# Kernel tuning notes

Hardware: AMD Instinct MI355X
Metric: run time of the kernel (lower is better)

Reference implementation:

```python
import jax, jax.numpy as jnp
import numpy as np
import math

B, S, N, D_IN = 32, 60, 25, 100
GRU, TEMB, SEMB, SEM_IN, CH, OUT, NH = 512, 512, 512, 768, 256, 512, 8


def _ln(x, g, b, eps=1e-5):
    m = jnp.mean(x, axis=-1, keepdims=True)
    v = jnp.mean((x - m) ** 2, axis=-1, keepdims=True)
    return (x - m) * jax.lax.rsqrt(v + eps) * g + b


def _gru_dir(x, w_ih, w_hh, b_ih, b_hh, reverse):
    # x: [BN, S, F]; PyTorch GRU gate order (r, z, n); returns final hidden [BN, H]
    H = w_hh.shape[1]
    gi_all = jnp.einsum('bsf,gf->bsg', x, w_ih) + b_ih  # precompute input-side gates

    def step(h, gi):
        gh = h @ w_hh.T + b_hh
        i_r, i_z, i_n = jnp.split(gi, 3, axis=-1)
        h_r, h_z, h_n = jnp.split(gh, 3, axis=-1)
        r = jax.nn.sigmoid(i_r + h_r)
        z = jax.nn.sigmoid(i_z + h_z)
        n = jnp.tanh(i_n + r * h_n)
        h_new = (1.0 - z) * n + z * h
        return h_new, None

    h0 = jnp.zeros((x.shape[0], H), x.dtype)
    h_last, _ = jax.lax.scan(step, h0, jnp.swapaxes(gi_all, 0, 1), reverse=reverse)
    return h_last


def _forward(x, seq1_w1, seq1_b1, seq1_w2, seq1_b2, ln2_g, ln2_b,
             gru_wih_f, gru_whh_f, gru_bih_f, gru_bhh_f,
             gru_wih_b, gru_whh_b, gru_bih_b, gru_bhh_b,
             ln_g, ln_b, attn_in_w, attn_in_b, fc_ta_w, fc_ta_b,
             ln3_g, ln3_b, semantic_embs, sem_w, sem_b, lnsem_g, lnsem_b,
             att_alpha, dist_adj,
             gcn_w0, gcn_b0, gcn_w1, gcn_b1, gcn_w2, gcn_b2,
             gln1_g, gln1_b, gln2_g, gln2_b,
             enc_ln_g, enc_ln_b, fc_w, fc_b):
    Bx, Sx, Nx, _ = x.shape
    # --- latent_correlation_layer ---
    xr = jnp.transpose(x, (0, 2, 1, 3)).reshape(Bx * Nx, Sx, -1)  # [BN,S,D]
    h = jax.nn.relu(xr @ seq1_w1 + seq1_b1)
    h = jax.nn.relu(h @ seq1_w2 + seq1_b2)  # dropout p=0
    h = _ln(h, ln2_g, ln2_b)  # [BN,S,512]
    hf = _gru_dir(h, gru_wih_f, gru_whh_f, gru_bih_f, gru_bhh_f, False)
    hb = _gru_dir(h, gru_wih_b, gru_whh_b, gru_bih_b, gru_bhh_b, True)
    hn = jnp.concatenate([hf, hb], axis=-1).reshape(Bx, Nx, 2 * GRU)
    hn = _ln(hn, ln_g, ln_b)  # [B,N,2*GRU]
    # multihead self-attention weights (averaged over heads, then over batch)
    hd = (2 * GRU) // NH
    qkv = hn @ attn_in_w.T + attn_in_b
    q, k, _v = jnp.split(qkv, 3, axis=-1)
    q = q.reshape(Bx, Nx, NH, hd)
    k = k.reshape(Bx, Nx, NH, hd)
    scores = jnp.einsum('bihd,bjhd->bhij', q, k) / math.sqrt(hd)
    attention = jax.nn.softmax(scores, axis=-1).mean(axis=1).mean(axis=0)  # [N,N]
    # --- node features ---
    wr = jax.nn.relu(hn @ fc_ta_w + fc_ta_b)
    X = _ln(wr, ln3_g, ln3_b)  # [B,N,TEMB]
    te = _ln(semantic_embs @ sem_w + sem_b, lnsem_g, lnsem_b)  # [N,SEMB]
    X = jnp.concatenate([X, jnp.broadcast_to(te, (Bx,) + te.shape)], axis=-1)  # [B,N,TEMB+SEMB]
    # cosine-similarity embedding attention (same for every batch element)
    en = te / jnp.maximum(jnp.linalg.norm(te, axis=-1, keepdims=True), 1e-8)
    embed_att = en @ en.T  # [N,N]
    attention = (att_alpha * dist_adj + (1.0 - att_alpha) * embed_att) * attention
    # case-amplification mask (detached in the original -> stop_gradient)
    m = jax.lax.stop_gradient(attention)
    m = jnp.maximum(m, 0.0) ** 2.5
    m = m / jnp.max(m)
    mask = (m >= 0.08).astype(x.dtype)
    adj = attention * mask
    # --- GCN block (GCNConv, add_self_loops=False, normalize=False, dense adjacency) ---
    def gcn(Xin, W, b):
        # out[i] = sum_j adj[j,i] * (Xin[j] @ W) + b  (source->target flow)
        return jnp.einsum('ji,bjf->bif', adj, Xin @ W) + b
    Xg = jax.nn.relu(gcn(X, gcn_w0, gcn_b0))
    Xg = jax.nn.relu(_ln(gcn(Xg, gcn_w1, gcn_b1) + Xg, gln1_g, gln1_b))
    Xg = jax.nn.relu(_ln(gcn(Xg, gcn_w2, gcn_b2) + Xg, gln2_g, gln2_b))
    # --- encoder head ---
    Xg = _ln(Xg, enc_ln_g, enc_ln_b)
    X_hat = jax.nn.relu(jnp.concatenate([X, Xg], axis=-1) @ fc_w + fc_b)  # [B,N,OUT]
    return X_hat


def setup_inputs():
    key = jax.random.key(0)
    c = [0]

    def nrm(shape, scale=1.0):
        c[0] += 1
        return (jax.random.normal(jax.random.fold_in(key, c[0]), shape) * scale).astype(jnp.float32)

    z = lambda *s: jnp.zeros(s, jnp.float32)
    o = lambda *s: jnp.ones(s, jnp.float32)
    FDIM = TEMB + SEMB
    d = {
        'x': nrm((B, S, N, D_IN)),
        'seq1_w1': nrm((D_IN, 256), 0.06), 'seq1_b1': z(256),
        'seq1_w2': nrm((256, 512), 0.05), 'seq1_b2': z(512),
        'ln2_g': o(512), 'ln2_b': z(512),
        'gru_wih_f': nrm((3 * GRU, 512), 0.04), 'gru_whh_f': nrm((3 * GRU, GRU), 0.04),
        'gru_bih_f': z(3 * GRU), 'gru_bhh_f': z(3 * GRU),
        'gru_wih_b': nrm((3 * GRU, 512), 0.04), 'gru_whh_b': nrm((3 * GRU, GRU), 0.04),
        'gru_bih_b': z(3 * GRU), 'gru_bhh_b': z(3 * GRU),
        'ln_g': o(2 * GRU), 'ln_b': z(2 * GRU),
        'attn_in_w': nrm((3 * 2 * GRU, 2 * GRU), 0.03), 'attn_in_b': z(3 * 2 * GRU),
        'fc_ta_w': nrm((2 * GRU, TEMB), 0.04), 'fc_ta_b': z(TEMB),
        'ln3_g': o(TEMB), 'ln3_b': z(TEMB),
        'semantic_embs': nrm((N, SEM_IN)),
        'sem_w': nrm((SEM_IN, SEMB), 0.04), 'sem_b': z(SEMB),
        'lnsem_g': o(SEMB), 'lnsem_b': z(SEMB),
        'att_alpha': jnp.float32(0.5),
        'dist_adj': jax.random.uniform(jax.random.fold_in(key, 1000), (N, N), jnp.float32),
        'gcn_w0': nrm((FDIM, CH), 0.04), 'gcn_b0': z(CH),
        'gcn_w1': nrm((CH, CH), 0.06), 'gcn_b1': z(CH),
        'gcn_w2': nrm((CH, CH), 0.06), 'gcn_b2': z(CH),
        'gln1_g': o(CH), 'gln1_b': z(CH),
        'gln2_g': o(CH), 'gln2_b': z(CH),
        'enc_ln_g': o(CH), 'enc_ln_b': z(CH),
        'fc_w': nrm((FDIM + CH, OUT), 0.04), 'fc_b': z(OUT),
    }
    return d


def reference(x, seq1_w1, seq1_b1, seq1_w2, seq1_b2, ln2_g, ln2_b,
              gru_wih_f, gru_whh_f, gru_bih_f, gru_bhh_f,
              gru_wih_b, gru_whh_b, gru_bih_b, gru_bhh_b,
              ln_g, ln_b, attn_in_w, attn_in_b, fc_ta_w, fc_ta_b,
              ln3_g, ln3_b, semantic_embs, sem_w, sem_b, lnsem_g, lnsem_b,
              att_alpha, dist_adj,
              gcn_w0, gcn_b0, gcn_w1, gcn_b1, gcn_w2, gcn_b2,
              gln1_g, gln1_b, gln2_g, gln2_b,
              enc_ln_g, enc_ln_b, fc_w, fc_b):
    return _forward(x, seq1_w1, seq1_b1, seq1_w2, seq1_b2, ln2_g, ln2_b,
                    gru_wih_f, gru_whh_f, gru_bih_f, gru_bhh_f,
                    gru_wih_b, gru_whh_b, gru_bih_b, gru_bhh_b,
                    ln_g, ln_b, attn_in_w, attn_in_b, fc_ta_w, fc_ta_b,
                    ln3_g, ln3_b, semantic_embs, sem_w, sem_b, lnsem_g, lnsem_b,
                    att_alpha, dist_adj,
                    gcn_w0, gcn_b0, gcn_w1, gcn_b1, gcn_w2, gcn_b2,
                    gln1_g, gln1_b, gln2_g, gln2_b,
                    enc_ln_g, enc_ln_b, fc_w, fc_b)
```

## Files before the change

### kernel.cpp

```cpp
#include <hip/hip_runtime.h>
#include <hip/hip_bf16.h>
#include <math.h>

#define BB 32
#define SS 60
#define NN_ 25
#define DIN 100
#define BN 800
#define GRU_H 512
#define FDIM 1024
#define CH 256
#define OUTD 512

typedef unsigned short ushort_t;
typedef unsigned int u32;
typedef unsigned long long u64;
typedef float f32x4 __attribute__((ext_vector_type(4)));
typedef __bf16 bf16x8 __attribute__((ext_vector_type(8)));
typedef short s16x8 __attribute__((ext_vector_type(8)));

static const size_t O_HSEQB = 0;
static const size_t O_WB    = 12288000;
static const size_t O_HF32  = 13860864;
static const size_t O_HRING = 14680064;
static const size_t O_HN    = 15908864;
static const size_t O_QKV   = 16728064;
static const size_t O_SC    = 18366464;
static const size_t O_ADJ   = 18530304;
static const size_t O_WR    = 18530944;
static const size_t O_TEP   = 18940544;
static const size_t O_TE    = 18953344;
static const size_t O_XCAT  = 18966144;
static const size_t O_GTMP  = 19990144;
static const size_t O_XG0   = 20194944;
static const size_t O_XG1   = 20399744;
static const size_t O_XG2   = 20604544;
static const size_t O_W1TB  = 20809344;
static const size_t O_W2TB  = 20825728;
static const size_t O_AWB   = 20891264;
static const size_t O_FTWB  = 21939840;
static const size_t O_SMWB  = 22201984;
static const size_t O_G0WB  = 22398592;
static const size_t O_G1WB  = 22529664;
static const size_t O_G2WB  = 22562432;
static const size_t O_FCWB  = 22595200;
static const size_t O_FLAGS = 22922880;

__device__ __forceinline__ ushort_t f2b(float v)
{
  __hip_bfloat16 b = __float2bfloat16(v);
  return *reinterpret_cast<ushort_t*>(&b);
}

__device__ __forceinline__ float sig_fast(float v)
{
  return 1.f / (1.f + __expf(-v));
}
__device__ __forceinline__ float tanh_fast(float v)
{
  return 1.f - 2.f / (1.f + __expf(2.f * v));
}

__device__ __forceinline__ void block_reduce2(float& s, float& q, float* scratch)
{
  __syncthreads();
  #pragma unroll
  for (int off = 32; off > 0; off >>= 1) {
    s += __shfl_down(s, off);
    q += __shfl_down(q, off);
  }
  int tid = threadIdx.x;
  int w = tid >> 6;
  if ((tid & 63) == 0) { scratch[w * 2] = s; scratch[w * 2 + 1] = q; }
  __syncthreads();
  if (tid == 0) {
    float ss = 0.f, qq = 0.f;
    int nw = blockDim.x >> 6;
    for (int i = 0; i < nw; i++) { ss += scratch[i * 2]; qq += scratch[i * 2 + 1]; }
    scratch[0] = ss; scratch[1] = qq;
  }
  __syncthreads();
  s = scratch[0]; q = scratch[1];
}

__global__ __launch_bounds__(256) void k_cvt_plain_all(
    const float* __restrict__ wih_f, const float* __restrict__ whh_f,
    const float* __restrict__ wih_b, const float* __restrict__ whh_b,
    const float* __restrict__ attn_w,
    ushort_t* __restrict__ wb, ushort_t* __restrict__ awb)
{
  int i = blockIdx.x * 256 + threadIdx.x;
  wb[i]           = f2b(wih_f[i]);
  wb[786432 + i]  = f2b(whh_f[i]);
  wb[1572864 + i] = f2b(wih_b[i]);
  wb[2359296 + i] = f2b(whh_b[i]);
  awb[i]          = f2b(attn_w[i]);
  awb[786432 + i] = f2b(attn_w[786432 + i]);
  int j = 1572864 + i;
  if (j < 2097152) awb[j] = f2b(attn_w[j]);
}

struct TJob {
  const float* src; ushort_t* dst;
  int K, N, KP, base;
};

__global__ __launch_bounds__(256) void k_cvt_t_all(
    TJob j0, TJob j1, TJob j2, TJob j3, TJob j4, TJob j5, TJob j6, TJob j7)
{
  __shared__ float tile[32][33];
  int t = blockIdx.x;
  TJob jb = j0;
  if (t >= j7.base) jb = j7;
  else if (t >= j6.base) jb = j6;
  else if (t >= j5.base) jb = j5;
  else if (t >= j4.base) jb = j4;
  else if (t >= j3.base) jb = j3;
  else if (t >= j2.base) jb = j2;
  else if (t >= j1.base) jb = j1;
  int local = t - jb.base;
  int ktiles = (jb.KP + 31) >> 5;
  int n0 = (local / ktiles) * 32;
  int k0 = (local % ktiles) * 32;
  int tx = threadIdx.x & 31, ty = threadIdx.x >> 5;
  #pragma unroll
  for (int i = 0; i < 4; i++) {
    int k = k0 + ty + i * 8, n = n0 + tx;
    tile[ty + i * 8][tx] = (k < jb.K && n < jb.N) ? jb.src[(size_t)k * jb.N + n] : 0.f;
  }
  __syncthreads();
  #pragma unroll
  for (int i = 0; i < 4; i++) {
    int n = n0 + ty + i * 8, k = k0 + tx;
    if (n < jb.N && k < jb.KP) jb.dst[(size_t)n * jb.KP + k] = f2b(tile[tx][ty + i * 8]);
  }
}

__global__ __launch_bounds__(256, 1) void k_mlp_fused(
    const float* __restrict__ x,
    const ushort_t* __restrict__ w1tb,
    const float* __restrict__ b1,
    const ushort_t* __restrict__ w2tb,
    const float* __restrict__ b2,
    const float* __restrict__ g, const float* __restrict__ be,
    ushort_t* __restrict__ hseqb)
{
  __shared__ __align__(16) ushort_t xb[64][136];
  __shared__ __align__(16) ushort_t Bl[512][40];
  __shared__ __align__(16) ushort_t h1[64][264];
  const int tid = threadIdx.x;
  const int r0 = blockIdx.x * 64;

  {
    int rr = tid >> 2;
    int d0 = (tid & 3) * 32;
    int r = r0 + rr;
    int bn = r / SS, s = r % SS;
    int b = bn / NN_, n = bn % NN_;
    const float* xp = x + (((size_t)b * SS + s) * NN_ + n) * DIN;
    ushort_t tmp[32];
    #pragma unroll
    for (int i = 0; i < 32; i++) {
      int d = d0 + i;
      tmp[i] = (d < DIN) ? f2b(xp[d]) : (ushort_t)0;
    }
    #pragma unroll
    for (int i = 0; i < 4; i++)
      *reinterpret_cast<s16x8*>(&xb[rr][d0 + i * 8]) = *reinterpret_cast<s16x8*>(&tmp[i * 8]);
  }
  const int wid = tid >> 6, l = tid & 63, lr = l & 15, lg = l >> 4;
  const int srow = tid >> 2, skg = (tid & 3) * 8;

  f32x4 acc1[16] = {};
  for (int kc = 0; kc < 4; kc++) {
    __syncthreads();
    #pragma unroll
    for (int i = 0; i < 4; i++) {
      int row = srow + i * 64;
      *reinterpret_cast<s16x8*>(&Bl[row][skg]) =
          *reinterpret_cast<const s16x8*>(w1tb + (size_t)row * 128 + kc * 32 + skg);
    }
    __syncthreads();
    bf16x8 aF = *reinterpret_cast<const bf16x8*>(&xb[wid * 16 + lr][kc * 32 + lg * 8]);
    #pragma unroll
    for (int ni = 0; ni < 16; ni++) {
      bf16x8 bF = *reinterpret_cast<const bf16x8*>(&Bl[ni * 16 + lr][lg * 8]);
      acc1[ni] = __builtin_amdgcn_mfma_f32_16x16x32_bf16(aF, bF, acc1[ni], 0, 0, 0);
    }
  }
  #pragma unroll
  for (int ni = 0; ni < 16; ni++) {
    #pragma unroll
    for (int r = 0; r < 4; r++) {
      int row = wid * 16 + lg * 4 + r;
      int col = ni * 16 + lr;
      h1[row][col] = f2b(fmaxf(acc1[ni][r] + b1[col], 0.f));
    }
  }

  f32x4 acc2[32] = {};
  for (int kc = 0; kc < 8; kc++) {
    __syncthreads();
    #pragma unroll
    for (int i = 0; i < 8; i++) {
      int row = srow + i * 64;
      *reinterpret_cast<s16x8*>(&Bl[row][skg]) =
          *reinterpret_cast<const s16x8*>(w2tb + (size_t)row * 256 + kc * 32 + skg);
    }
    __syncthreads();
    bf16x8 aF = *reinterpret_cast<const bf16x8*>(&h1[wid * 16 + lr][kc * 32 + lg * 8]);
    #pragma unroll
    for (int ni = 0; ni < 32; ni++) {
      bf16x8 bF = *reinterpret_cast<const bf16x8*>(&Bl[ni * 16 + lr][lg * 8]);
      acc2[ni] = __builtin_amdgcn_mfma_f32_16x16x32_bf16(aF, bF, acc2[ni], 0, 0, 0);
    }
  }

  float su[4] = {0.f, 0.f, 0.f, 0.f}, sq[4] = {0.f, 0.f, 0.f, 0.f};
  #pragma unroll
  for (int ni = 0; ni < 32; ni++) {
    float bb = b2[ni * 16 + lr];
    #pragma unroll
    for (int r = 0; r < 4; r++) {
      float v = fmaxf(acc2[ni][r] + bb, 0.f);
      acc2[ni][r] = v;
      su[r] += v; sq[r] += v * v;
    }
  }
  #pragma unroll
  for (int off = 1; off < 16; off <<= 1) {
    #pragma unroll
    for (int r = 0; r < 4; r++) {
      su[r] += __shfl_xor(su[r], off);
      sq[r] += __shfl_xor(sq[r], off);
    }
  }
  #pragma unroll
  for (int r = 0; r < 4; r++) {
    float mean = su[r] * (1.f / 512.f);
    float var = sq[r] * (1.f / 512.f) - mean * mean;
    float rs = rsqrtf(var + 1e-5f);
    int rowg = r0 + wid * 16 + lg * 4 + r;
    ushort_t* outp = hseqb + (size_t)rowg * 512;
    #pragma unroll
    for (int ni = 0; ni < 32; ni++) {
      int col = ni * 16 + lr;
      outp[col] = f2b((acc2[ni][r] - mean) * rs * g[col] + be[col]);
    }
  }
}

__global__ __launch_bounds__(256, 1) void k_gru_persist(
    const ushort_t* __restrict__ hseqb, const ushort_t* __restrict__ wb,
    const float* __restrict__ bih_f, const float* __restrict__ bhh_f,
    const float* __restrict__ bih_b, const float* __restrict__ bhh_b,
    float* __restrict__ hf32, ushort_t* __restrict__ hring,
    int* __restrict__ flags)
{
  __shared__ __align__(16) ushort_t Xf[64][520];
  __shared__ __align__(16) ushort_t Hf[64][520];
  __shared__ __align__(16) ushort_t hpack[64][72];
  __shared__ int s_item;

  const int tid = threadIdx.x;

  int* qcnt = flags + 448;
  if (tid == 0) {
    u32 xcc;
    asm volatile("s_getreg_b32 %0, hwreg(HW_REG_XCC_ID)" : "=s"(xcc));
    xcc &= 7u;
    int idx = __hip_atomic_fetch_add(qcnt + xcc, 1, __ATOMIC_RELAXED,
                                     __HIP_MEMORY_SCOPE_AGENT);
    s_item = (idx << 3) | (int)xcc;
  }
  __syncthreads();
  const int xcd = s_item & 7;
  const int idx = s_item >> 3;
  const int x3 = xcd & 3;
  const int dir = xcd >> 2;
  const int nmt = (x3 == 0) ? 4 : 3;
  if (idx >= nmt * 8) return;
  const int mt = (idx >> 3) * 4 + x3;
  const int jt = idx & 7;
  const int j0g = jt * 64;
  const int m0g = mt * 64;
  const int chain = dir * 13 + mt;
  int* flagp = flags + chain * 16;

  const ushort_t* __restrict__ wih = wb + (size_t)dir * 1572864;
  const ushort_t* __restrict__ whh = wih + 786432;
  const float* __restrict__ bih = dir ? bih_b : bih_f;
  const float* __restrict__ bhh = dir ? bhh_b : bhh_f;
  const size_t dirOff = (size_t)dir * 409600;

  const int srow = tid >> 2;
  const int skg  = (tid & 3) * 8;
  const int smg  = m0g + srow;
  const int smg_c = (smg < BN) ? smg : 0;

  const int wid = tid >> 6;
  const int l = tid & 63;
  const int lr = l & 15;
  const int lg = l >> 4;
  const int jg = j0g + (wid << 4) + lr;

  const ushort_t* pwf[6];
  #pragma unroll
  for (int tt = 0; tt < 6; tt++) {
    const ushort_t* src = (tt < 3) ? wih : whh;
    int gate = (tt < 3) ? tt : tt - 3;
    pwf[tt] = src + ((size_t)(gate * 512 + jg) * 512) + lg * 8;
  }

  const float rbr  = bih[jg] + bhh[jg];
  const float rbz  = bih[512 + jg] + bhh[512 + jg];
  const float rbin = bih[1024 + jg];
  const float rbhn = bhh[1024 + jg];

  float hpreg[4][4] = {};

  for (int t = 0; t < SS; ++t) {
    const int xt = dir ? (SS - 1 - t) : t;
    const ushort_t* __restrict__ hprev = hring + (size_t)(t % 3) * 819200 + dirOff;
    ushort_t* __restrict__ hnew = hring + (size_t)((t + 1) % 3) * 819200 + dirOff;
    const ushort_t* __restrict__ px = hseqb + ((size_t)smg_c * SS + xt) * 512 + skg;

    s16x8 rxv[16];
    #pragma unroll
    for (int c = 0; c < 16; c++)
      rxv[c] = *reinterpret_cast<const s16x8*>(px + c * 32);

    if (t > 0 && tid == 0) {
      while (__hip_atomic_load(flagp, __ATOMIC_RELAXED, __HIP_MEMORY_SCOPE_SYSTEM) < 8 * t) {
        __builtin_amdgcn_s_sleep(2);
      }
    }
    __syncthreads();

    {
      const ushort_t* ph = hprev + (size_t)smg_c * 512 + skg;
      u64 hv[32];
      #pragma unroll
      for (int c = 0; c < 16; c++) {
        hv[2 * c]     = *reinterpret_cast<const volatile u64*>(ph + c * 32);
        hv[2 * c + 1] = *reinterpret_cast<const volatile u64*>(ph + c * 32 + 4);
      }
      #pragma unroll
      for (int c = 0; c < 16; c++) {
        *reinterpret_cast<s16x8*>(&Xf[srow][c * 32 + skg]) = rxv[c];
        *reinterpret_cast<u64*>(&Hf[srow][c * 32 + skg])     = hv[2 * c];
        *reinterpret_cast<u64*>(&Hf[srow][c * 32 + skg + 4]) = hv[2 * c + 1];
      }
    }
    __syncthreads();

    f32x4 accr[4] = {};
    f32x4 accz[4] = {};
    f32x4 accin[4] = {};
    f32x4 acchn[4] = {};

    #pragma unroll 4
    for (int it = 0; it < 16; ++it) {
      const int k0 = it * 32;
      bf16x8 bW[6];
      #pragma unroll
      for (int tt = 0; tt < 6; tt++)
        bW[tt] = *reinterpret_cast<const bf16x8*>(pwf[tt] + k0);
      bf16x8 xA[4], hA[4];
      #pragma unroll
      for (int mi = 0; mi < 4; mi++) {
        xA[mi] = *reinterpret_cast<const bf16x8*>(&Xf[mi * 16 + lr][k0 + lg * 8]);
        hA[mi] = *reinterpret_cast<const bf16x8*>(&Hf[mi * 16 + lr][k0 + lg * 8]);
      }
      #pragma unroll
      for (int mi = 0; mi < 4; mi++) {
        accr[mi]  = __builtin_amdgcn_mfma_f32_16x16x32_bf16(xA[mi], bW[0], accr[mi], 0, 0, 0);
        accr[mi]  = __builtin_amdgcn_mfma_f32_16x16x32_bf16(hA[mi], bW[3], accr[mi], 0, 0, 0);
        accz[mi]  = __builtin_amdgcn_mfma_f32_16x16x32_bf16(xA[mi], bW[1], accz[mi], 0, 0, 0);
        accz[mi]  = __builtin_amdgcn_mfma_f32_16x16x32_bf16(hA[mi], bW[4], accz[mi], 0, 0, 0);
        accin[mi] = __builtin_amdgcn_mfma_f32_16x16x32_bf16(xA[mi], bW[2], accin[mi], 0, 0, 0);
        acchn[mi] = __builtin_amdgcn_mfma_f32_16x16x32_bf16(hA[mi], bW[5], acchn[mi], 0, 0, 0);
      }
    }

    #pragma unroll
    for (int mi = 0; mi < 4; mi++) {
      #pragma unroll
      for (int r = 0; r < 4; r++) {
        float sr = accr[mi][r] + rbr;
        float sz = accz[mi][r] + rbz;
        float rg = sig_fast(sr);
        float zg = sig_fast(sz);
        float ng = tanh_fast(accin[mi][r] + rbin + rg * (acchn[mi][r] + rbhn));
        hpreg[mi][r] = (1.f - zg) * ng + zg * hpreg[mi][r];
      }
    }

    if (t < SS - 1) {
      #pragma unroll
      for (int mi = 0; mi < 4; mi++)
        #pragma unroll
        for (int r = 0; r < 4; r++)
          hpack[mi * 16 + lg * 4 + r][(wid << 4) + lr] = f2b(hpreg[mi][r]);
      __syncthreads();
      {
        int row = tid >> 2;
        int gm = m0g + row;
        if (gm < BN) {
          ushort_t* dst = hnew + (size_t)gm * 512 + j0g + (tid & 3) * 16;
          *reinterpret_cast<s16x8*>(dst) =
              *reinterpret_cast<s16x8*>(&hpack[row][(tid & 3) * 16]);
          *reinterpret_cast<s16x8*>(dst + 8) =
              *reinterpret_cast<s16x8*>(&hpack[row][(tid & 3) * 16 + 8]);
        }
      }
      __syncthreads();
      if (tid == 0)
        __hip_atomic_fetch_add(flagp, 1, __ATOMIC_RELAXED, __HIP_MEMORY_SCOPE_SYSTEM);
    } else {
      float* hfin = hf32 + dirOff;
      #pragma unroll
      for (int mi = 0; mi < 4; mi++) {
        #pragma unroll
        for (int r = 0; r < 4; r++) {
          int m = m0g + mi * 16 + lg * 4 + r;
          if (m < BN) hfin[(size_t)m * 512 + jg] = hpreg[mi][r];
        }
      }
    }
  }
}

__global__ __launch_bounds__(256) void k_ln_hn(
    const float* __restrict__ hf, const float* __restrict__ hb,
    const float* __restrict__ g, const float* __restrict__ be,
    float* __restrict__ hn)
{
  __shared__ float scratch[8];
  int row = blockIdx.x, tid = threadIdx.x;
  float v[4];
  float s = 0.f, q = 0.f;
  #pragma unroll
  for (int p = 0; p < 4; p++) {
    int c = p * 256 + tid;
    float val = (c < 512) ? hf[(size_t)row * 512 + c] : hb[(size_t)row * 512 + (c - 512)];
    v[p] = val; s += val; q += val * val;
  }
  block_reduce2(s, q, scratch);
  float mean = s * (1.f / 1024.f);
  float var = q * (1.f / 1024.f) - mean * mean;
  float rs = rsqrtf(var + 1e-5f);
  #pragma unroll
  for (int p = 0; p < 4; p++) {
    int c = p * 256 + tid;
    hn[(size_t)row * 1024 + c] = (v[p] - mean) * rs * g[c] + be[c];
  }
}

template<int ACT>
__global__ __launch_bounds__(256) void k_bgemm(
    const float* __restrict__ A, const ushort_t* __restrict__ B,
    const float* __restrict__ bias, float* __restrict__ C,
    int M, int N, int K, int lda, int ldc)
{
  __shared__ __align__(16) ushort_t Al[64][40];
  __shared__ __align__(16) ushort_t Bl[64][40];
  const int tid = threadIdx.x;
  const int n0g = blockIdx.x * 64, m0g = blockIdx.y * 64;
  const int srow = tid >> 2, skg = (tid & 3) * 8;
  const int smg = (m0g + srow < M) ? (m0g + srow) : (M - 1);
  const int sng = (n0g + srow < N) ? (n0g + srow) : (N - 1);
  const float* pa = A + (size_t)smg * lda + skg;
  const ushort_t* pb = B + (size_t)sng * K + skg;
  const int wid = tid >> 6, l = tid & 63, lr = l & 15, lg = l >> 4;
  const int mbase = (wid >> 1) * 32, nbase = (wid & 1) * 32;
  f32x4 acc[2][2] = {};

  for (int k0 = 0; k0 < K; k0 += 32) {
    float4 a0 = *reinterpret_cast<const float4*>(pa + k0);
    float4 a1 = *reinterpret_cast<const float4*>(pa + k0 + 4);
    s16x8 bv = *reinterpret_cast<const s16x8*>(pb + k0);
    ushort_t tmp[8] = {f2b(a0.x), f2b(a0.y), f2b(a0.z), f2b(a0.w),
                       f2b(a1.x), f2b(a1.y), f2b(a1.z), f2b(a1.w)};
    *reinterpret_cast<s16x8*>(&Al[srow][skg]) = *reinterpret_cast<s16x8*>(tmp);
    *reinterpret_cast<s16x8*>(&Bl[srow][skg]) = bv;
    __syncthreads();
    bf16x8 aF[2], bF[2];
    #pragma unroll
    for (int mi = 0; mi < 2; mi++)
      aF[mi] = *reinterpret_cast<const bf16x8*>(&Al[mbase + mi * 16 + lr][lg * 8]);
    #pragma unroll
    for (int ni = 0; ni < 2; ni++)
      bF[ni] = *reinterpret_cast<const bf16x8*>(&Bl[nbase + ni * 16 + lr][lg * 8]);
    #pragma unroll
    for (int mi = 0; mi < 2; mi++)
      #pragma unroll
      for (int ni = 0; ni < 2; ni++)
        acc[mi][ni] = __builtin_amdgcn_mfma_f32_16x16x32_bf16(aF[mi], bF[ni], acc[mi][ni], 0, 0, 0);
    __syncthreads();
  }
  #pragma unroll
  for (int mi = 0; mi < 2; mi++) {
    #pragma unroll
    for (int r = 0; r < 4; r++) {
      int mg = m0g + mbase + mi * 16 + lg * 4 + r;
      if (mg >= M) continue;
      #pragma unroll
      for (int ni = 0; ni < 2; ni++) {
        int ng = n0g + nbase + ni * 16 + lr;
        if (ng >= N) continue;
        float v = acc[mi][ni][r] + (bias ? bias[ng] : 0.f);
        if (ACT == 1) v = fmaxf(v, 0.f);
        C[(size_t)mg * ldc + ng] = v;
      }
    }
  }
}

__global__ __launch_bounds__(256) void k_scores(const float* __restrict__ qkv,
                                                float* __restrict__ sc)
{
  int b = blockIdx.x, h = blockIdx.y;
  __shared__ float qs[25][128];
  __shared__ float ks[25][129];
  __shared__ float ps[25][26];
  int tid = threadIdx.x;
  for (int idx = tid; idx < 3200; idx += 256) {
    int i = idx >> 7, d = idx & 127;
    const float* base = qkv + (size_t)(b * 25 + i) * 2048 + h * 128 + d;
    qs[i][d] = base[0];
    ks[i][d] = base[1024];
  }
  __syncthreads();
  const float scale = 0.08838834764831845f;
  for (int e = tid; e < 625; e += 256) {
    int i = e / 25, j = e % 25;
    float s = 0.f;
    for (int d = 0; d < 128; d++) s += qs[i][d] * ks[j][d];
    ps[i][j] = s * scale;
  }
  __syncthreads();
  if (tid < 25) {
    float mx = -1e30f;
    for (int j = 0; j < 25; j++) mx = fmaxf(mx, ps[tid][j]);
    float s = 0.f;
    for (int j = 0; j < 25; j++) { float ev = expf(ps[tid][j] - mx); ps[tid][j] = ev; s += ev; }
    float inv = 1.f / s;
    for (int j = 0; j < 25; j++) ps[tid][j] *= inv;
  }
  __syncthreads();
  float* out = sc + (size_t)(b * 8 + h) * 640;
  for (int e = tid; e < 625; e += 256) out[e] = ps[e / 25][e % 25];
}

template<int PER>
__global__ __launch_bounds__(256) void k_ln_rows(
    const float* __restrict__ src, float* __restrict__ dst,
    const float* __restrict__ g, const float* __restrict__ be,
    int dstStride, int dstOff)
{
  __shared__ float scratch[8];
  int row = blockIdx.x, tid = threadIdx.x;
  const int C = PER * 256;
  float v[PER];
  float s = 0.f, q = 0.f;
  #pragma unroll
  for (int p = 0; p < PER; p++) {
    v[p] = src[(size_t)row * C + p * 256 + tid];
    s += v[p]; q += v[p] * v[p];
  }
  block_reduce2(s, q, scratch);
  float mean = s / (float)C;
  float var = q / (float)C - mean * mean;
  float rs = rsqrtf(var + 1e-5f);
  #pragma unroll
  for (int p = 0; p < PER; p++) {
    int c = p * 256 + tid;
    dst[(size_t)row * dstStride + dstOff + c] = (v[p] - mean) * rs * g[c] + be[c];
  }
}

__global__ __launch_bounds__(256) void k_bcast_te(const float* __restrict__ te,
                                                  float* __restrict__ xcat)
{
  int row = blockIdx.x, tid = threadIdx.x;
  int n = row % 25;
  xcat[(size_t)row * 1280 + 512 + tid] = te[n * 512 + tid];
  xcat[(size_t)row * 1280 + 768 + tid] = te[n * 512 + 256 + tid];
}

__global__ __launch_bounds__(1024) void k_adj(
    const float* __restrict__ sc, const float* __restrict__ te,
    const float* __restrict__ alpha_p, const float* __restrict__ dist,
    float* __restrict__ adj)
{
  __shared__ float tes[25][517];
  __shared__ float als[625];
  __shared__ float dots[625];
  __shared__ float scratch[16];
  __shared__ float mxs;
  int tid = threadIdx.x;

  for (int idx = tid; idx < 12800; idx += 1024)
    tes[idx >> 9][idx & 511] = te[idx];
  __syncthreads();

  if (tid < 625) {
    int i = tid / 25, j = tid % 25;
    float s = 0.f;
    for (int gq = 0; gq < 256; gq++) s += sc[(size_t)gq * 640 + tid];
    als[tid] = s * (1.f / 256.f);
    float dt = 0.f;
    const float* ti = tes[i];
    const float* tj = tes[j];
    for (int d = 0; d < 512; d++) dt += ti[d] * tj[d];
    dots[tid] = dt;
  }
  __syncthreads();
  float alpha = alpha_p[0];
  float lm = 0.f;
  if (tid < 625) {
    int i = tid / 25, j = tid % 25;
    float ni = 1.f / fmaxf(sqrtf(dots[i * 26]), 1e-8f);
    float nj = 1.f / fmaxf(sqrtf(dots[j * 26]), 1e-8f);
    float emb = dots[tid] * ni * nj;
    float a = (alpha * dist[tid] + (1.f - alpha) * emb) * als[tid];
    als[tid] = a;
    lm = powf(fmaxf(a, 0.f), 2.5f);
  }
  #pragma unroll
  for (int off = 32; off > 0; off >>= 1) lm = fmaxf(lm, __shfl_down(lm, off));
  int w = tid >> 6;
  if ((tid & 63) == 0) scratch[w] = lm;
  __syncthreads();
  if (tid == 0) {
    float m2 = scratch[0];
    for (int i = 1; i < 16; i++) m2 = fmaxf(m2, scratch[i]);
    mxs = m2;
  }
  __syncthreads();
  if (tid < 625) {
    float a = als[tid];
    float m = powf(fmaxf(a, 0.f), 2.5f) / mxs;
    adj[tid] = (m >= 0.08f) ? a : 0.f;
  }
}

template<int RESID, int LNORM>
__global__ __launch_bounds__(256) void k_mix(
    const float* __restrict__ adj, const float* __restrict__ tmp,
    const float* __restrict__ bias, const float* __restrict__ resid,
    const float* __restrict__ g, const float* __restrict__ be,
    float* __restrict__ out)
{
  __shared__ float adjs[25];
  __shared__ float scratch[8];
  int row = blockIdx.x;
  int b = row / 25, i = row % 25;
  int f = threadIdx.x;
  if (f < 25) adjs[f] = adj[f * 25 + i];
  __syncthreads();
  float acc = bias[f];
  const float* tp = tmp + (size_t)b * 25 * 256 + f;
  #pragma unroll 5
  for (int j = 0; j < 25; j++) acc += adjs[j] * tp[(size_t)j * 256];
  if (RESID) acc += resid[(size_t)row * 256 + f];
  float v = acc;
  if (LNORM) {
    float s = v, q = v * v;
    block_reduce2(s, q, scratch);
    float mean = s * (1.f / 256.f);
    float var = q * (1.f / 256.f) - mean * mean;
    v = (v - mean) * rsqrtf(var + 1e-5f) * g[f] + be[f];
  }
  out[(size_t)row * 256 + f] = fmaxf(v, 0.f);
}

extern "C" void kernel_launch(void* const* d_in, const int* in_sizes, int n_in,
                              void* d_out, int out_size, void* d_ws, size_t ws_size,
                              hipStream_t stream)
{
  (void)in_sizes; (void)n_in; (void)out_size; (void)ws_size;

  const float* x         = (const float*)d_in[0];
  const float* seq1_w1   = (const float*)d_in[1];
  const float* seq1_b1   = (const float*)d_in[2];
  const float* seq1_w2   = (const float*)d_in[3];
  const float* seq1_b2   = (const float*)d_in[4];
  const float* ln2_g     = (const float*)d_in[5];
  const float* ln2_b     = (const float*)d_in[6];
  const float* gru_wih_f = (const float*)d_in[7];
  const float* gru_whh_f = (const float*)d_in[8];
  const float* gru_bih_f = (const float*)d_in[9];
  const float* gru_bhh_f = (const float*)d_in[10];
  const float* gru_wih_b = (const float*)d_in[11];
  const float* gru_whh_b = (const float*)d_in[12];
  const float* gru_bih_b = (const float*)d_in[13];
  const float* gru_bhh_b = (const float*)d_in[14];
  const float* ln_g      = (const float*)d_in[15];
  const float* ln_b      = (const float*)d_in[16];
  const float* attn_in_w = (const float*)d_in[17];
  const float* attn_in_b = (const float*)d_in[18];
  const float* fc_ta_w   = (const float*)d_in[19];
  const float* fc_ta_b   = (const float*)d_in[20];
  const float* ln3_g     = (const float*)d_in[21];
  const float* ln3_b     = (const float*)d_in[22];
  const float* sem_embs  = (const float*)d_in[23];
  const float* sem_w     = (const float*)d_in[24];
  const float* sem_b     = (const float*)d_in[25];
  const float* lnsem_g   = (const float*)d_in[26];
  const float* lnsem_b   = (const float*)d_in[27];
  const float* att_alpha = (const float*)d_in[28];
  const float* dist_adj  = (const float*)d_in[29];
  const float* gcn_w0    = (const float*)d_in[30];
  const float* gcn_b0    = (const float*)d_in[31];
  const float* gcn_w1    = (const float*)d_in[32];
  const float* gcn_b1    = (const float*)d_in[33];
  const float* gcn_w2    = (const float*)d_in[34];
  const float* gcn_b2    = (const float*)d_in[35];
  const float* gln1_g    = (const float*)d_in[36];
  const float* gln1_b    = (const float*)d_in[37];
  const float* gln2_g    = (const float*)d_in[38];
  const float* gln2_b    = (const float*)d_in[39];
  const float* enc_ln_g  = (const float*)d_in[40];
  const float* enc_ln_b  = (const float*)d_in[41];
  const float* fc_w      = (const float*)d_in[42];
  const float* fc_b      = (const float*)d_in[43];

  float* w = (float*)d_ws;
  ushort_t* hseqb = (ushort_t*)(w + O_HSEQB);
  ushort_t* wb    = (ushort_t*)(w + O_WB);
  float* hf32 = w + O_HF32;
  ushort_t* hring = (ushort_t*)(w + O_HRING);
  float* hn   = w + O_HN;
  float* qkv  = w + O_QKV;
  float* sc   = w + O_SC;
  float* adjw = w + O_ADJ;
  float* wr   = w + O_WR;
  float* tep  = w + O_TEP;
  float* te   = w + O_TE;
  float* xcat = w + O_XCAT;
  float* gtmp = w + O_GTMP;
  float* xg0  = w + O_XG0;
  float* xg1  = w + O_XG1;
  float* xg2  = w + O_XG2;
  ushort_t* w1tb = (ushort_t*)(w + O_W1TB);
  ushort_t* w2tb = (ushort_t*)(w + O_W2TB);
  ushort_t* awb  = (ushort_t*)(w + O_AWB);
  ushort_t* ftwb = (ushort_t*)(w + O_FTWB);
  ushort_t* smwb = (ushort_t*)(w + O_SMWB);
  ushort_t* g0wb = (ushort_t*)(w + O_G0WB);
  ushort_t* g1wb = (ushort_t*)(w + O_G1WB);
  ushort_t* g2wb = (ushort_t*)(w + O_G2WB);
  ushort_t* fcwb = (ushort_t*)(w + O_FCWB);
  int* flags = (int*)(w + O_FLAGS);

  hipMemsetAsync(hring, 0, (size_t)819200 * sizeof(ushort_t), stream);
  hipMemsetAsync(flags, 0, 512 * sizeof(int), stream);

  k_cvt_plain_all<<<3072, 256, 0, stream>>>(gru_wih_f, gru_whh_f, gru_wih_b,
                                            gru_whh_b, attn_in_w, wb, awb);
  {
    TJob j0 = {seq1_w1, w1tb, 100, 256, 128, 0};
    TJob j1 = {seq1_w2, w2tb, 256, 512, 256, 32};
    TJob j2 = {fc_ta_w, ftwb, 1024, 512, 1024, 160};
    TJob j3 = {sem_w, smwb, 768, 512, 768, 672};
    TJob j4 = {gcn_w0, g0wb, 1024, 256, 1024, 1056};
    TJob j5 = {gcn_w1, g1wb, 256, 256, 256, 1312};
    TJob j6 = {gcn_w2, g2wb, 256, 256, 256, 1376};
    TJob j7 = {fc_w, fcwb, 1280, 512, 1280, 1440};
    k_cvt_t_all<<<2080, 256, 0, stream>>>(j0, j1, j2, j3, j4, j5, j6, j7);
  }

  k_mlp_fused<<<750, 256, 0, stream>>>(x, w1tb, seq1_b1, w2tb, seq1_b2,
                                       ln2_g, ln2_b, hseqb);

  k_gru_persist<<<256, 256, 0, stream>>>(
      hseqb, wb, gru_bih_f, gru_bhh_f, gru_bih_b, gru_bhh_b, hf32, hring, flags);

  k_ln_hn<<<800, 256, 0, stream>>>(hf32, hf32 + 409600, ln_g, ln_b, hn);

  k_bgemm<0><<<dim3(32, 13), 256, 0, stream>>>(
      hn, awb, attn_in_b, qkv, 800, 2048, 1024, 1024, 2048);

  k_scores<<<dim3(32, 8), 256, 0, stream>>>(qkv, sc);

  k_bgemm<0><<<dim3(8, 1), 256, 0, stream>>>(
      sem_embs, smwb, sem_b, tep, 25, 512, 768, 768, 512);
  k_ln_rows<2><<<25, 256, 0, stream>>>(tep, te, lnsem_g, lnsem_b, 512, 0);

  k_bgemm<1><<<dim3(8, 13), 256, 0, stream>>>(
      hn, ftwb, fc_ta_b, wr, 800, 512, 1024, 1024, 512);
  k_ln_rows<2><<<800, 256, 0, stream>>>(wr, xcat, ln3_g, ln3_b, 1280, 0);
  k_bcast_te<<<800, 256, 0, stream>>>(te, xcat);

  k_adj<<<1, 1024, 0, stream>>>(sc, te, att_alpha, dist_adj, adjw);

  k_bgemm<0><<<dim3(4, 13), 256, 0, stream>>>(
      xcat, g0wb, nullptr, gtmp, 800, 256, 1024, 1280, 256);
  k_mix<0, 0><<<800, 256, 0, stream>>>(adjw, gtmp, gcn_b0, nullptr, nullptr, nullptr, xg0);
  k_bgemm<0><<<dim3(4, 13), 256, 0, stream>>>(
      xg0, g1wb, nullptr, gtmp, 800, 256, 256, 256, 256);
  k_mix<1, 1><<<800, 256, 0, stream>>>(adjw, gtmp, gcn_b1, xg0, gln1_g, gln1_b, xg1);
  k_bgemm<0><<<dim3(4, 13), 256, 0, stream>>>(
      xg1, g2wb, nullptr, gtmp, 800, 256, 256, 256, 256);
  k_mix<1, 1><<<800, 256, 0, stream>>>(adjw, gtmp, gcn_b2, xg1, gln2_g, gln2_b, xg2);

  k_ln_rows<1><<<800, 256, 0, stream>>>(xg2, xcat, enc_ln_g, enc_ln_b, 1280, 1024);

  k_bgemm<1><<<dim3(8, 13), 256, 0, stream>>>(
      xcat, fcwb, fc_b, (float*)d_out, 800, 512, 1280, 1280, 512);
}
```

Before: 1.454 ms.

## Split GRU persistent kernel into narrower 32-column tiles across 512 blocks

The persistent GRU kernel now splits each 64-row chain into 16 column tiles of 32 hidden units instead of 8 tiles of 64, launching 512 blocks at two blocks per CU. The x-side A fragments are loaded straight from global memory rather than staged through shared memory, which removes the Xf buffer and shrinks hpack. The aim is more parallelism and a shorter per-step critical path for the 60 sequential steps. In exchange each chain has twice as many producers to synchronise, the flag spin becomes a plain volatile load, and the flag increment is relaxed to workgroup scope. That scope is weaker than needed for cross-block visibility and risks stale reads of the hidden-state ring.

```diff
diff --git a/kernel.cpp b/kernel.cpp
--- a/kernel.cpp
+++ b/kernel.cpp
@@ -250,16 +250,15 @@
   }
 }
 
-__global__ __launch_bounds__(256, 1) void k_gru_persist(
+__global__ __launch_bounds__(256, 2) void k_gru_persist(
     const ushort_t* __restrict__ hseqb, const ushort_t* __restrict__ wb,
     const float* __restrict__ bih_f, const float* __restrict__ bhh_f,
     const float* __restrict__ bih_b, const float* __restrict__ bhh_b,
     float* __restrict__ hf32, ushort_t* __restrict__ hring,
     int* __restrict__ flags)
 {
-  __shared__ __align__(16) ushort_t Xf[64][520];
   __shared__ __align__(16) ushort_t Hf[64][520];
-  __shared__ __align__(16) ushort_t hpack[64][72];
+  __shared__ __align__(16) ushort_t hpack[64][36];
   __shared__ int s_item;
 
   const int tid = threadIdx.x;
@@ -276,13 +275,13 @@
   __syncthreads();
   const int xcd = s_item & 7;
   const int idx = s_item >> 3;
+  if (idx >= 64) return;
   const int x3 = xcd & 3;
   const int dir = xcd >> 2;
-  const int nmt = (x3 == 0) ? 4 : 3;
-  if (idx >= nmt * 8) return;
-  const int mt = (idx >> 3) * 4 + x3;
-  const int jt = idx & 7;
-  const int j0g = jt * 64;
+  const int jt = idx & 15;
+  const int mt = (idx >> 4) * 4 + x3;
+  if (mt >= 13) return;
+  const int j0g = jt * 32;
   const int m0g = mt * 64;
   const int chain = dir * 13 + mt;
   int* flagp = flags + chain * 16;
@@ -302,7 +301,8 @@
   const int l = tid & 63;
   const int lr = l & 15;
   const int lg = l >> 4;
-  const int jg = j0g + (wid << 4) + lr;
+  const int mbase = (wid >> 1) * 32;
+  const int jg = j0g + (wid & 1) * 16 + lr;
 
   const ushort_t* pwf[6];
   #pragma unroll
@@ -312,26 +312,32 @@
     pwf[tt] = src + ((size_t)(gate * 512 + jg) * 512) + lg * 8;
   }
 
+  int xrow[2];
+  #pragma unroll
+  for (int mi = 0; mi < 2; mi++) {
+    int m = m0g + mbase + mi * 16 + lr;
+    xrow[mi] = (m < BN) ? m : (BN - 1);
+  }
+
   const float rbr  = bih[jg] + bhh[jg];
   const float rbz  = bih[512 + jg] + bhh[512 + jg];
   const float rbin = bih[1024 + jg];
   const float rbhn = bhh[1024 + jg];
 
-  float hpreg[4][4] = {};
+  float hpreg[2][4] = {};
 
   for (int t = 0; t < SS; ++t) {
     const int xt = dir ? (SS - 1 - t) : t;
     const ushort_t* __restrict__ hprev = hring + (size_t)(t % 3) * 819200 + dirOff;
     ushort_t* __restrict__ hnew = hring + (size_t)((t + 1) % 3) * 819200 + dirOff;
-    const ushort_t* __restrict__ px = hseqb + ((size_t)smg_c * SS + xt) * 512 + skg;
-
-    s16x8 rxv[16];
-    #pragma unroll
-    for (int c = 0; c < 16; c++)
-      rxv[c] = *reinterpret_cast<const s16x8*>(px + c * 32);
+
+    const ushort_t* pxf[2];
+    #pragma unroll
+    for (int mi = 0; mi < 2; mi++)
+      pxf[mi] = hseqb + ((size_t)xrow[mi] * SS + xt) * 512 + lg * 8;
 
     if (t > 0 && tid == 0) {
-      while (__hip_atomic_load(flagp, __ATOMIC_RELAXED, __HIP_MEMORY_SCOPE_SYSTEM) < 8 * t) {
+      while (*(volatile const int*)flagp < 16 * t) {
         __builtin_amdgcn_s_sleep(2);
       }
     }
@@ -347,17 +353,16 @@
       }
       #pragma unroll
       for (int c = 0; c < 16; c++) {
-        *reinterpret_cast<s16x8*>(&Xf[srow][c * 32 + skg]) = rxv[c];
         *reinterpret_cast<u64*>(&Hf[srow][c * 32 + skg])     = hv[2 * c];
         *reinterpret_cast<u64*>(&Hf[srow][c * 32 + skg + 4]) = hv[2 * c + 1];
       }
     }
     __syncthreads();
 
-    f32x4 accr[4] = {};
-    f32x4 accz[4] = {};
-    f32x4 accin[4] = {};
-    f32x4 acchn[4] = {};
+    f32x4 accr[2] = {};
+    f32x4 accz[2] = {};
+    f32x4 accin[2] = {};
+    f32x4 acchn[2] = {};
 
     #pragma unroll 4
     for (int it = 0; it < 16; ++it) {
@@ -366,14 +371,14 @@
       #pragma unroll
       for (int tt = 0; tt < 6; tt++)
         bW[tt] = *reinterpret_cast<const bf16x8*>(pwf[tt] + k0);
-      bf16x8 xA[4], hA[4];
-      #pragma unroll
-      for (int mi = 0; mi < 4; mi++) {
-        xA[mi] = *reinterpret_cast<const bf16x8*>(&Xf[mi * 16 + lr][k0 + lg * 8]);
-        hA[mi] = *reinterpret_cast<const bf16x8*>(&Hf[mi * 16 + lr][k0 + lg * 8]);
+      bf16x8 xA[2], hA[2];
+      #pragma unroll
+      for (int mi = 0; mi < 2; mi++) {
+        xA[mi] = *reinterpret_cast<const bf16x8*>(pxf[mi] + k0);
+        hA[mi] = *reinterpret_cast<const bf16x8*>(&Hf[mbase + mi * 16 + lr][k0 + lg * 8]);
       }
       #pragma unroll
-      for (int mi = 0; mi < 4; mi++) {
+      for (int mi = 0; mi < 2; mi++) {
         accr[mi]  = __builtin_amdgcn_mfma_f32_16x16x32_bf16(xA[mi], bW[0], accr[mi], 0, 0, 0);
         accr[mi]  = __builtin_amdgcn_mfma_f32_16x16x32_bf16(hA[mi], bW[3], accr[mi], 0, 0, 0);
         accz[mi]  = __builtin_amdgcn_mfma_f32_16x16x32_bf16(xA[mi], bW[1], accz[mi], 0, 0, 0);
@@ -384,7 +389,7 @@
     }
 
     #pragma unroll
-    for (int mi = 0; mi < 4; mi++) {
+    for (int mi = 0; mi < 2; mi++) {
       #pragma unroll
       for (int r = 0; r < 4; r++) {
         float sr = accr[mi][r] + rbr;
@@ -398,32 +403,30 @@
 
     if (t < SS - 1) {
       #pragma unroll
-      for (int mi = 0; mi < 4; mi++)
+      for (int mi = 0; mi < 2; mi++)
         #pragma unroll
         for (int r = 0; r < 4; r++)
-          hpack[mi * 16 + lg * 4 + r][(wid << 4) + lr] = f2b(hpreg[mi][r]);
+          hpack[mbase + mi * 16 + lg * 4 + r][(wid & 1) * 16 + lr] = f2b(hpreg[mi][r]);
       __syncthreads();
       {
         int row = tid >> 2;
         int gm = m0g + row;
         if (gm < BN) {
-          ushort_t* dst = hnew + (size_t)gm * 512 + j0g + (tid & 3) * 16;
+          ushort_t* dst = hnew + (size_t)gm * 512 + j0g + (tid & 3) * 8;
           *reinterpret_cast<s16x8*>(dst) =
-              *reinterpret_cast<s16x8*>(&hpack[row][(tid & 3) * 16]);
-          *reinterpret_cast<s16x8*>(dst + 8) =
-              *reinterpret_cast<s16x8*>(&hpack[row][(tid & 3) * 16 + 8]);
+              *reinterpret_cast<s16x8*>(&hpack[row][(tid & 3) * 8]);
         }
       }
       __syncthreads();
       if (tid == 0)
-        __hip_atomic_fetch_add(flagp, 1, __ATOMIC_RELAXED, __HIP_MEMORY_SCOPE_SYSTEM);
+        __hip_atomic_fetch_add(flagp, 1, __ATOMIC_RELAXED, __HIP_MEMORY_SCOPE_WORKGROUP);
     } else {
       float* hfin = hf32 + dirOff;
       #pragma unroll
-      for (int mi = 0; mi < 4; mi++) {
+      for (int mi = 0; mi < 2; mi++) {
         #pragma unroll
         for (int r = 0; r < 4; r++) {
-          int m = m0g + mi * 16 + lg * 4 + r;
+          int m = m0g + mbase + mi * 16 + lg * 4 + r;
           if (m < BN) hfin[(size_t)m * 512 + jg] = hpreg[mi][r];
         }
       }
@@ -775,7 +778,7 @@
   k_mlp_fused<<<750, 256, 0, stream>>>(x, w1tb, seq1_b1, w2tb, seq1_b2,
                                        ln2_g, ln2_b, hseqb);
 
-  k_gru_persist<<<256, 256, 0, stream>>>(
+  k_gru_persist<<<512, 256, 0, stream>>>(
       hseqb, wb, gru_bih_f, gru_bhh_f, gru_bih_b, gru_bhh_b, hf32, hring, flags);
 
   k_ln_hn<<<800, 256, 0, stream>>>(hf32, hf32 + 409600, ln_g, ln_b, hn);
```

Result: slower. 2.399 ms (median of 4 runs) (+65.0%).
